# Optimization experiments

Hardware: AMD Instinct MI355X
Metric: run time of the kernel (lower is better)

## Reference

```python
import jax, jax.numpy as jnp
import numpy as np

CONF = 0.25
IOU = 0.7
MAX_DET = 300
IMG_H = 1280
IMG_W = 1280
KPT_SHAPE = (17, 3)
MAX_NMS = 3000
BS = 16
N_ANCH = 33600  # (1280/8)^2 + (1280/16)^2 + (1280/32)^2


def setup_inputs() -> dict:
    key = jax.random.key(0)
    k1, k2, k3, k4 = jax.random.split(key, 4)
    # realistic YOLO head outputs: centers in image, positive w/h, conf in (0,1)
    cxy = jax.random.uniform(k1, (BS, 2, N_ANCH)) * jnp.array([IMG_W, IMG_H], jnp.float32).reshape(1, 2, 1)
    wh = jax.random.uniform(k2, (BS, 2, N_ANCH)) * 200.0 + 4.0
    conf = jax.random.uniform(k3, (BS, 1, N_ANCH))
    kpts = jax.random.uniform(k4, (BS, 51, N_ANCH)) * float(IMG_W)
    preds = jnp.concatenate([cxy, wh, conf, kpts], axis=1).astype(jnp.float32)
    return {"preds": preds}


def _pairwise_iou(boxes):
    # boxes: [M, 4] xyxy
    area = (boxes[:, 2] - boxes[:, 0]) * (boxes[:, 3] - boxes[:, 1])
    lt = jnp.maximum(boxes[:, None, :2], boxes[None, :, :2])
    rb = jnp.minimum(boxes[:, None, 2:], boxes[None, :, 2:])
    wh = jnp.clip(rb - lt, 0.0)
    inter = wh[..., 0] * wh[..., 1]
    return inter / (area[:, None] + area[None, :] - inter + 1e-9)


def _nms_keep(boxes, valid):
    # greedy NMS over score-descending boxes; returns bool keep mask [M]
    M = boxes.shape[0]
    idx = jnp.arange(M)
    supp = (_pairwise_iou(boxes) > IOU) & (idx[None, :] > idx[:, None])

    def body(i, keep):
        # row i suppresses later boxes only if it is itself kept
        return keep & ~(supp[i] & keep[i])

    return jax.lax.fori_loop(0, M, body, valid)


def _per_image(boxes_xywh, scores, kpts):
    # boxes_xywh: [N,4], scores: [N], kpts: [N,51]
    valid = scores > CONF
    masked = jnp.where(valid, scores, -1.0)
    order = jnp.argsort(-masked)[:MAX_NMS]  # top max_nms by score, desc
    b = boxes_xywh[order]
    sc = scores[order]
    kp = kpts[order]
    v = valid[order]
    # xywh -> xyxy with clip to image bounds
    cx, cy, w, h = b[:, 0], b[:, 1], b[:, 2], b[:, 3]
    x1 = jnp.clip(cx - w / 2, 0.0, IMG_W)
    y1 = jnp.clip(cy - h / 2, 0.0, IMG_H)
    x2 = jnp.clip(cx + w / 2, 0.0, IMG_W)
    y2 = jnp.clip(cy + h / 2, 0.0, IMG_H)
    bxy = jnp.stack([x1, y1, x2, y2], axis=-1)
    # faithful to original _clip_coords quirk: only channels 0 and 1 of the 51 clipped
    kp = kp.at[:, 0].set(jnp.clip(kp[:, 0], 0.0, IMG_W))
    kp = kp.at[:, 1].set(jnp.clip(kp[:, 1], 0.0, IMG_H))
    keep = _nms_keep(bxy, v)
    rank = jnp.cumsum(keep) - 1
    sel = keep & (rank < MAX_DET)
    tgt = jnp.where(sel, rank, MAX_DET)  # dropped rows scatter to slot MAX_DET (sliced off)
    ob = jnp.zeros((MAX_DET + 1, 4), bxy.dtype).at[tgt].set(jnp.where(sel[:, None], bxy, 0.0))[:MAX_DET]
    osc = jnp.zeros((MAX_DET + 1, 1), sc.dtype).at[tgt].set(jnp.where(sel[:, None], sc[:, None], 0.0))[:MAX_DET]
    okp = jnp.zeros((MAX_DET + 1, 51), kp.dtype).at[tgt].set(jnp.where(sel[:, None], kp, 0.0))[:MAX_DET]
    return ob, osc, okp


def reference(preds):
    bs = preds.shape[0]
    x = jnp.transpose(preds, (0, 2, 1))  # [bs, N, 56]
    ob, osc, okp = jax.vmap(_per_image)(x[..., :4], x[..., 4], x[..., 5:])
    return ob, osc, okp.reshape(bs, MAX_DET, *KPT_SHAPE)
```

## Files before the change

kernel.cpp:

```cpp
#include <hip/hip_runtime.h>
#include <stdint.h>

#define N_ANCH 33600
#define BS 16
#define NCH 56
#define MAX_NMS 3000
#define MAX_DET 300
#define CONF_T 0.25f
#define IOU_T 0.7f
#define IMG 1280.0f
#define NW 47
#define NBINS 4096
#define HIST_BINS 4097
#define CAP 4096
#define WCAP 4096
#define WC_STRIDE 16

#define OFF_CAND 0
#define OFF_WL   (OFF_CAND + BS*CAP*8)
#define OFF_WC   (OFF_WL + BS*WCAP*4)
#define OFF_KEPT (OFF_WC + BS*WC_STRIDE*4)
#define OFF_OIDX (OFF_KEPT + 64)
#define OFF_SC   (OFF_OIDX + BS*MAX_NMS*4)
#define OFF_SEL  (OFF_SC + BS*MAX_NMS*4)
#define OFF_BOX  (((OFF_SEL + BS*MAX_DET*4) + 15) & ~15)

__device__ __forceinline__ int score_bucket(float c, uint32_t* bits_out) {
    if (!(c > CONF_T)) { *bits_out = 0u; return 0; }
    uint32_t bits = __float_as_uint(c);
    *bits_out = bits;
    int bucket = (int)(bits >> 12) - 0x3E800 + 1;
    bucket = bucket < 1 ? 1 : (bucket > NBINS ? NBINS : bucket);
    return bucket;
}

__global__ void k_phase1(const float* __restrict__ preds,
                         unsigned long long* __restrict__ cand,
                         unsigned int* __restrict__ wlist, int* __restrict__ wcount,
                         int* __restrict__ oidx, float* __restrict__ sc_out,
                         float4* __restrict__ box_out) {
    __shared__ int hl[HIST_BINS];
    __shared__ int st[HIST_BINS];
    __shared__ int part[256];
    __shared__ int suf[256];
    __shared__ int ldsB, ldsM, ldsWc;
    int b = blockIdx.x, t = threadIdx.x;
    if (t == 0) { ldsWc = 0; }
    for (int i = t; i < HIST_BINS; i += 1024) hl[i] = 0;
    __syncthreads();
    const float4* conf4 = (const float4*)(preds + (size_t)b * NCH * N_ANCH + 4 * N_ANCH);
    for (int a4 = t; a4 < N_ANCH / 4; a4 += 1024) {
        float4 c4 = conf4[a4];
        uint32_t bits;
        int bk;
        bk = score_bucket(c4.x, &bits); if (bk > 0) atomicAdd(&hl[bk], 1);
        bk = score_bucket(c4.y, &bits); if (bk > 0) atomicAdd(&hl[bk], 1);
        bk = score_bucket(c4.z, &bits); if (bk > 0) atomicAdd(&hl[bk], 1);
        bk = score_bucket(c4.w, &bits); if (bk > 0) atomicAdd(&hl[bk], 1);
    }
    __syncthreads();
    if (t < 256) {
        int s = 0;
        for (int k = 0; k < 16; k++) s += hl[1 + t * 16 + k];
        part[t] = s;
    }
    __syncthreads();
    if (t == 0) {
        int run = 0;
        for (int i = 255; i >= 0; i--) { suf[i] = run; run += part[i]; }
        if (run < MAX_NMS) { ldsB = 1; ldsM = run; }
    }
    __syncthreads();
    if (t < 256) {
        int run = suf[t];
        bool maycross = (run < MAX_NMS) && (run + part[t] >= MAX_NMS);
        bool done = false;
        for (int k = 15; k >= 0; k--) {
            int bin = 1 + t * 16 + k;
            st[bin] = run;
            run += hl[bin];
            if (maycross && !done && run >= MAX_NMS) { ldsB = bin; ldsM = run; done = true; }
        }
    }
    __syncthreads();
    int B = ldsB, M = ldsM;
    if (t < 256) {
        for (int k = 0; k < 16; k++) {
            int bin = 1 + t * 16 + k;
            int c = hl[bin], s = st[bin];
            if (c > 0 && bin >= B && s < MAX_NMS) {
                int idx = atomicAdd(&ldsWc, 1);
                wlist[b * WCAP + idx] = (unsigned int)s | ((unsigned int)c << 16);
            }
        }
    }
    __syncthreads();
    for (int a4 = t; a4 < N_ANCH / 4; a4 += 1024) {
        float4 c4 = conf4[a4];
        float cv[4] = {c4.x, c4.y, c4.z, c4.w};
        #pragma unroll
        for (int q = 0; q < 4; q++) {
            uint32_t bits;
            int bucket = score_bucket(cv[q], &bits);
            if (bucket >= B && bucket > 0) {
                int pos = atomicAdd(&st[bucket], 1);
                if (pos < CAP) {
                    int a = a4 * 4 + q;
                    cand[b * CAP + pos] =
                        ((unsigned long long)bits << 32) | (uint32_t)(~(uint32_t)a);
                }
            }
        }
    }
    for (int p = M + t; p < MAX_NMS; p += 1024) {
        sc_out[b * MAX_NMS + p] = -1.0f;
        box_out[b * MAX_NMS + p] = make_float4(0.f, 0.f, 0.f, 0.f);
        oidx[b * MAX_NMS + p] = 0;
    }
    if (t == 0) wcount[b * WC_STRIDE] = ldsWc;
}

__global__ void k_rank2(const float* __restrict__ preds,
                        const unsigned long long* __restrict__ cand,
                        const unsigned int* __restrict__ wlist,
                        const int* __restrict__ wcount,
                        int* __restrict__ oidx, float* __restrict__ sc_out,
                        float4* __restrict__ box_out) {
    int b = blockIdx.x;
    int wc = wcount[b * WC_STRIDE];
    int wv = blockIdx.y * (blockDim.x >> 6) + (threadIdx.x >> 6);
    int lane = threadIdx.x & 63;
    const int wstride = gridDim.y * (blockDim.x >> 6);
    const float* pr = preds + (size_t)b * NCH * N_ANCH;
    for (int e = wv; e < wc; e += wstride) {
        unsigned int ent = wlist[b * WCAP + e];
        int s = (int)(ent & 0xffffu);
        int n = (int)(ent >> 16);
        if (s + n > CAP) n = CAP - s;
        const unsigned long long* seg = cand + b * CAP + s;
        for (int i = lane; i < n; i += 64) {
            unsigned long long ke = seg[i];
            int r = 0;
            for (int j = 0; j < n; j++) r += (seg[j] > ke);
            int pos = s + r;
            if (pos < MAX_NMS) {
                int oi = (int)(~(uint32_t)ke);
                float score = __uint_as_float((uint32_t)(ke >> 32));
                float cx = pr[0 * N_ANCH + oi], cy = pr[1 * N_ANCH + oi];
                float w  = pr[2 * N_ANCH + oi], h  = pr[3 * N_ANCH + oi];
                float4 bx;
                bx.x = fminf(fmaxf(cx - w * 0.5f, 0.f), IMG);
                bx.y = fminf(fmaxf(cy - h * 0.5f, 0.f), IMG);
                bx.z = fminf(fmaxf(cx + w * 0.5f, 0.f), IMG);
                bx.w = fminf(fmaxf(cy + h * 0.5f, 0.f), IMG);
                oidx[b * MAX_NMS + pos] = oi;
                sc_out[b * MAX_NMS + pos] = score;
                box_out[b * MAX_NMS + pos] = bx;
            }
        }
    }
}

__device__ __forceinline__ float iou_pair(float4 bi, float ai, float4 bj) {
    float aj  = (bj.z - bj.x) * (bj.w - bj.y);
    float ltx = fmaxf(bi.x, bj.x), lty = fmaxf(bi.y, bj.y);
    float rbx = fminf(bi.z, bj.z), rby = fminf(bi.w, bj.w);
    float wx  = fmaxf(rbx - ltx, 0.f), wy = fmaxf(rby - lty, 0.f);
    float inter = wx * wy;
    return inter / (ai + aj - inter + 1e-9f);
}

__device__ __forceinline__ unsigned long long readlane64(unsigned long long v, int lane) {
    uint32_t lo = (uint32_t)v, hi = (uint32_t)(v >> 32);
    uint32_t rlo = __builtin_amdgcn_readlane(lo, lane);
    uint32_t rhi = __builtin_amdgcn_readlane(hi, lane);
    return ((unsigned long long)rhi << 32) | (unsigned long long)rlo;
}

__global__ void k_nms(const float4* __restrict__ box_ws, const float* __restrict__ sc_ws,
                      int* __restrict__ sel_slot, int* __restrict__ kept_count,
                      float* __restrict__ out) {
    __shared__ float4 lbox[MAX_NMS];
    __shared__ float4 kbox[MAX_DET];
    __shared__ float  karea[MAX_DET];
    __shared__ int    lsel[MAX_DET];
    __shared__ unsigned long long pres[NW];
    __shared__ unsigned long long diag[64];
    __shared__ unsigned long long keptmask_sh;
    int b = blockIdx.x, t = threadIdx.x;
    if (t < NW) pres[t] = 0ull;
    __syncthreads();
    for (int j = t; j < MAX_NMS; j += 1024) {
        lbox[j] = box_ws[b * MAX_NMS + j];
        if (!(sc_ws[b * MAX_NMS + j] > CONF_T))
            atomicOr(&pres[j >> 6], 1ull << (j & 63));
    }
    __syncthreads();
    int kc = 0;
    for (int c = 0; c < NW && kc < MAX_DET; c++) {
        int base = c * 64;
        if (t < 64) diag[t] = 0ull;
        __syncthreads();
        {
            int jl = t >> 4, kk = t & 15;
            int j = base + jl;
            if (j < MAX_NMS && kc > 0) {
                float4 bj = lbox[j];
                bool sup = false;
                for (int kidx = kk; kidx < kc; kidx += 16) {
                    if (iou_pair(kbox[kidx], karea[kidx], bj) > IOU_T) { sup = true; break; }
                }
                if (sup) atomicOr(&pres[c], 1ull << jl);
            }
        }
        {
            int il = t >> 4;
            int j0 = (t & 15) * 4;
            int i = base + il;
            if (i < MAX_NMS) {
                float4 bi = lbox[i];
                float ai = (bi.z - bi.x) * (bi.w - bi.y);
                unsigned long long m = 0ull;
                for (int q = 0; q < 4; q++) {
                    int jl = j0 + q, j = base + jl;
                    if (j > i && j < MAX_NMS) {
                        if (iou_pair(bi, ai, lbox[j]) > IOU_T) m |= 1ull << jl;
                    }
                }
                if (m) atomicOr(&diag[il], m);
            }
        }
        __syncthreads();
        if (t < 64) {
            unsigned long long mydiag = diag[t];
            unsigned long long s = pres[c];
            unsigned long long keptm = 0ull;
            int room = MAX_DET - kc;
            int jmax = MAX_NMS - base; if (jmax > 64) jmax = 64;
            for (int bb = 0; bb < jmax; bb++) {
                if (!((s >> bb) & 1ull)) {
                    s |= readlane64(mydiag, bb);
                    keptm |= 1ull << bb;
                    if (--room == 0) break;
                }
            }
            if (t == 0) keptmask_sh = keptm;
        }
        __syncthreads();
        unsigned long long keptm = keptmask_sh;
        if (t < 64 && ((keptm >> t) & 1ull)) {
            int pos = kc + __popcll(keptm & ((1ull << t) - 1ull));
            float4 bx = lbox[base + t];
            kbox[pos] = bx;
            karea[pos] = (bx.z - bx.x) * (bx.w - bx.y);
            lsel[pos] = base + t;
        }
        kc += __popcll(keptm);
        __syncthreads();
    }
    if (t == 0) kept_count[b] = kc;
    float* ob  = out;
    float* osc = out + BS * MAX_DET * 4;
    for (int r = t; r < MAX_DET; r += 1024) {
        int det = b * MAX_DET + r;
        if (r < kc) {
            float4 bx = kbox[r];
            ob[det * 4 + 0] = bx.x; ob[det * 4 + 1] = bx.y;
            ob[det * 4 + 2] = bx.z; ob[det * 4 + 3] = bx.w;
            osc[det] = sc_ws[b * MAX_NMS + lsel[r]];
            sel_slot[b * MAX_DET + r] = lsel[r];
        } else {
            ob[det * 4 + 0] = 0.f; ob[det * 4 + 1] = 0.f;
            ob[det * 4 + 2] = 0.f; ob[det * 4 + 3] = 0.f;
            osc[det] = 0.f;
        }
    }
}

__global__ void k_kpt(const float* __restrict__ preds, const int* __restrict__ oidx_ws,
                      const int* __restrict__ sel_slot, const int* __restrict__ kept_count,
                      float* __restrict__ out) {
    int g = blockIdx.x * blockDim.x + threadIdx.x;
    int det = g >> 6, lane = g & 63;
    if (det >= BS * MAX_DET || lane >= 51) return;
    int b = det / MAX_DET, r = det - b * MAX_DET;
    float* okp = out + BS * MAX_DET * 5;
    if (r < kept_count[b]) {
        int s = sel_slot[b * MAX_DET + r];
        int oi = oidx_ws[b * MAX_NMS + s];
        float v = preds[(size_t)b * NCH * N_ANCH + (size_t)(5 + lane) * N_ANCH + oi];
        if (lane < 2) v = fminf(fmaxf(v, 0.f), IMG);
        okp[det * 51 + lane] = v;
    } else {
        okp[det * 51 + lane] = 0.f;
    }
}

extern "C" void kernel_launch(void* const* d_in, const int* in_sizes, int n_in,
                              void* d_out, int out_size, void* d_ws, size_t ws_size,
                              hipStream_t stream) {
    const float* preds = (const float*)d_in[0];
    float* out = (float*)d_out;
    char* ws = (char*)d_ws;
    unsigned long long* cand = (unsigned long long*)(ws + OFF_CAND);
    unsigned int* wlist = (unsigned int*)(ws + OFF_WL);
    int* wcount = (int*)(ws + OFF_WC);
    int* kept = (int*)(ws + OFF_KEPT);
    int* oidx = (int*)(ws + OFF_OIDX);
    float* sc = (float*)(ws + OFF_SC);
    int* sel = (int*)(ws + OFF_SEL);
    float4* box = (float4*)(ws + OFF_BOX);

    k_phase1<<<BS, 1024, 0, stream>>>(preds, cand, wlist, wcount, oidx, sc, box);
    k_rank2<<<dim3(BS, 32), 256, 0, stream>>>(preds, cand, wlist, wcount, oidx, sc, box);
    k_nms<<<BS, 1024, 0, stream>>>(box, sc, sel, kept, out);
    k_kpt<<<(BS * MAX_DET * 64 + 255) / 256, 256, 0, stream>>>(preds, oidx, sel, kept, out);
}
```

Baseline: 231.5 us.

## Fuse histogram select, rank, and NMS into one per-image kernel

Merges the candidate histogram, in-bucket ranking, and greedy NMS into a single 1024-thread block per image. Boxes are now written straight into shared memory instead of a global workspace. Score and anchor index are packed into one meta array, and the final anchor index per detection is written out so the keypoint kernel needs a single indirection. This removes two kernel launches and several global round trips. In exchange, the ranking/gather stage runs on only 16 blocks instead of a wider grid, and shared memory is reused by aliasing the histogram region.

```diff
diff --git a/kernel.cpp b/kernel.cpp
--- a/kernel.cpp
+++ b/kernel.cpp
@@ -14,16 +14,11 @@
 #define HIST_BINS 4097
 #define CAP 4096
 #define WCAP 4096
-#define WC_STRIDE 16
 
 #define OFF_CAND 0
 #define OFF_WL   (OFF_CAND + BS*CAP*8)
-#define OFF_WC   (OFF_WL + BS*WCAP*4)
-#define OFF_KEPT (OFF_WC + BS*WC_STRIDE*4)
-#define OFF_OIDX (OFF_KEPT + 64)
-#define OFF_SC   (OFF_OIDX + BS*MAX_NMS*4)
-#define OFF_SEL  (OFF_SC + BS*MAX_NMS*4)
-#define OFF_BOX  (((OFF_SEL + BS*MAX_DET*4) + 15) & ~15)
+#define OFF_META (OFF_WL + BS*WCAP*4)
+#define OFF_FOI  (OFF_META + BS*MAX_NMS*8)
 
 __device__ __forceinline__ int score_bucket(float c, uint32_t* bits_out) {
     if (!(c > CONF_T)) { *bits_out = 0u; return 0; }
@@ -34,20 +29,48 @@
     return bucket;
 }
 
-__global__ void k_phase1(const float* __restrict__ preds,
-                         unsigned long long* __restrict__ cand,
-                         unsigned int* __restrict__ wlist, int* __restrict__ wcount,
-                         int* __restrict__ oidx, float* __restrict__ sc_out,
-                         float4* __restrict__ box_out) {
-    __shared__ int hl[HIST_BINS];
-    __shared__ int st[HIST_BINS];
-    __shared__ int part[256];
-    __shared__ int suf[256];
+__device__ __forceinline__ float iou_pair(float4 bi, float ai, float4 bj) {
+    float aj  = (bj.z - bj.x) * (bj.w - bj.y);
+    float ltx = fmaxf(bi.x, bj.x), lty = fmaxf(bi.y, bj.y);
+    float rbx = fminf(bi.z, bj.z), rby = fminf(bi.w, bj.w);
+    float wx  = fmaxf(rbx - ltx, 0.f), wy = fmaxf(rby - lty, 0.f);
+    float inter = wx * wy;
+    return inter / (ai + aj - inter + 1e-9f);
+}
+
+__device__ __forceinline__ unsigned long long readlane64(unsigned long long v, int lane) {
+    uint32_t lo = (uint32_t)v, hi = (uint32_t)(v >> 32);
+    uint32_t rlo = __builtin_amdgcn_readlane(lo, lane);
+    uint32_t rhi = __builtin_amdgcn_readlane(hi, lane);
+    return ((unsigned long long)rhi << 32) | (unsigned long long)rlo;
+}
+
+__global__ void __launch_bounds__(1024)
+k_fused(const float* __restrict__ preds,
+        unsigned long long* __restrict__ cand,
+        unsigned int* __restrict__ wlist,
+        uint2* __restrict__ meta,
+        int* __restrict__ foi,
+        float* __restrict__ out) {
+    __shared__ __align__(16) char sraw[48000];
+    float4* lbox = (float4*)sraw;
+    int* hl   = (int*)sraw;
+    int* st   = (int*)(sraw + 16388);
+    int* part = (int*)(sraw + 32776);
+    int* suf  = (int*)(sraw + 33800);
+    __shared__ float4 kbox[MAX_DET];
+    __shared__ float  karea[MAX_DET];
+    __shared__ int    lsel[MAX_DET];
+    __shared__ unsigned long long pres[NW];
+    __shared__ unsigned long long diag[64];
+    __shared__ unsigned long long keptmask_sh;
     __shared__ int ldsB, ldsM, ldsWc;
-    int b = blockIdx.x, t = threadIdx.x;
-    if (t == 0) { ldsWc = 0; }
+
+    const int b = blockIdx.x, t = threadIdx.x;
+    if (t == 0) ldsWc = 0;
     for (int i = t; i < HIST_BINS; i += 1024) hl[i] = 0;
     __syncthreads();
+
     const float4* conf4 = (const float4*)(preds + (size_t)b * NCH * N_ANCH + 4 * N_ANCH);
     for (int a4 = t; a4 < N_ANCH / 4; a4 += 1024) {
         float4 c4 = conf4[a4];
@@ -59,6 +82,7 @@
         bk = score_bucket(c4.w, &bits); if (bk > 0) atomicAdd(&hl[bk], 1);
     }
     __syncthreads();
+
     if (t < 256) {
         int s = 0;
         for (int k = 0; k < 16; k++) s += hl[1 + t * 16 + k];
@@ -83,7 +107,8 @@
         }
     }
     __syncthreads();
-    int B = ldsB, M = ldsM;
+    const int B = ldsB, M = ldsM;
+
     if (t < 256) {
         for (int k = 0; k < 16; k++) {
             int bin = 1 + t * 16 + k;
@@ -95,6 +120,7 @@
         }
     }
     __syncthreads();
+
     for (int a4 = t; a4 < N_ANCH / 4; a4 += 1024) {
         float4 c4 = conf4[a4];
         float cv[4] = {c4.x, c4.y, c4.z, c4.w};
@@ -112,90 +138,49 @@
             }
         }
     }
-    for (int p = M + t; p < MAX_NMS; p += 1024) {
-        sc_out[b * MAX_NMS + p] = -1.0f;
-        box_out[b * MAX_NMS + p] = make_float4(0.f, 0.f, 0.f, 0.f);
-        oidx[b * MAX_NMS + p] = 0;
-    }
-    if (t == 0) wcount[b * WC_STRIDE] = ldsWc;
-}
-
-__global__ void k_rank2(const float* __restrict__ preds,
-                        const unsigned long long* __restrict__ cand,
-                        const unsigned int* __restrict__ wlist,
-                        const int* __restrict__ wcount,
-                        int* __restrict__ oidx, float* __restrict__ sc_out,
-                        float4* __restrict__ box_out) {
-    int b = blockIdx.x;
-    int wc = wcount[b * WC_STRIDE];
-    int wv = blockIdx.y * (blockDim.x >> 6) + (threadIdx.x >> 6);
-    int lane = threadIdx.x & 63;
-    const int wstride = gridDim.y * (blockDim.x >> 6);
-    const float* pr = preds + (size_t)b * NCH * N_ANCH;
-    for (int e = wv; e < wc; e += wstride) {
-        unsigned int ent = wlist[b * WCAP + e];
-        int s = (int)(ent & 0xffffu);
-        int n = (int)(ent >> 16);
-        if (s + n > CAP) n = CAP - s;
-        const unsigned long long* seg = cand + b * CAP + s;
-        for (int i = lane; i < n; i += 64) {
-            unsigned long long ke = seg[i];
-            int r = 0;
-            for (int j = 0; j < n; j++) r += (seg[j] > ke);
-            int pos = s + r;
-            if (pos < MAX_NMS) {
-                int oi = (int)(~(uint32_t)ke);
-                float score = __uint_as_float((uint32_t)(ke >> 32));
-                float cx = pr[0 * N_ANCH + oi], cy = pr[1 * N_ANCH + oi];
-                float w  = pr[2 * N_ANCH + oi], h  = pr[3 * N_ANCH + oi];
-                float4 bx;
-                bx.x = fminf(fmaxf(cx - w * 0.5f, 0.f), IMG);
-                bx.y = fminf(fmaxf(cy - h * 0.5f, 0.f), IMG);
-                bx.z = fminf(fmaxf(cx + w * 0.5f, 0.f), IMG);
-                bx.w = fminf(fmaxf(cy + h * 0.5f, 0.f), IMG);
-                oidx[b * MAX_NMS + pos] = oi;
-                sc_out[b * MAX_NMS + pos] = score;
-                box_out[b * MAX_NMS + pos] = bx;
-            }
-        }
-    }
-}
-
-__device__ __forceinline__ float iou_pair(float4 bi, float ai, float4 bj) {
-    float aj  = (bj.z - bj.x) * (bj.w - bj.y);
-    float ltx = fmaxf(bi.x, bj.x), lty = fmaxf(bi.y, bj.y);
-    float rbx = fminf(bi.z, bj.z), rby = fminf(bi.w, bj.w);
-    float wx  = fmaxf(rbx - ltx, 0.f), wy = fmaxf(rby - lty, 0.f);
-    float inter = wx * wy;
-    return inter / (ai + aj - inter + 1e-9f);
-}
-
-__device__ __forceinline__ unsigned long long readlane64(unsigned long long v, int lane) {
-    uint32_t lo = (uint32_t)v, hi = (uint32_t)(v >> 32);
-    uint32_t rlo = __builtin_amdgcn_readlane(lo, lane);
-    uint32_t rhi = __builtin_amdgcn_readlane(hi, lane);
-    return ((unsigned long long)rhi << 32) | (unsigned long long)rlo;
-}
-
-__global__ void k_nms(const float4* __restrict__ box_ws, const float* __restrict__ sc_ws,
-                      int* __restrict__ sel_slot, int* __restrict__ kept_count,
-                      float* __restrict__ out) {
-    __shared__ float4 lbox[MAX_NMS];
-    __shared__ float4 kbox[MAX_DET];
-    __shared__ float  karea[MAX_DET];
-    __shared__ int    lsel[MAX_DET];
-    __shared__ unsigned long long pres[NW];
-    __shared__ unsigned long long diag[64];
-    __shared__ unsigned long long keptmask_sh;
-    int b = blockIdx.x, t = threadIdx.x;
-    if (t < NW) pres[t] = 0ull;
-    __syncthreads();
-    for (int j = t; j < MAX_NMS; j += 1024) {
-        lbox[j] = box_ws[b * MAX_NMS + j];
-        if (!(sc_ws[b * MAX_NMS + j] > CONF_T))
-            atomicOr(&pres[j >> 6], 1ull << (j & 63));
-    }
-    __syncthreads();
+    __syncthreads();
+
+    for (int p = M + t; p < MAX_NMS; p += 1024) lbox[p] = make_float4(0.f, 0.f, 0.f, 0.f);
+    if (t < NW) {
+        int base = t * 64;
+        int lo = M - base;
+        unsigned long long inv = (lo <= 0) ? ~0ull : (lo >= 64 ? 0ull : ~((1ull << lo) - 1ull));
+        pres[t] = inv;
+    }
+
+    {
+        const int wv = t >> 6, lane = t & 63;
+        const int wc = ldsWc;
+        const float* pr = preds + (size_t)b * NCH * N_ANCH;
+        for (int e = wv; e < wc; e += 16) {
+            unsigned int ent = wlist[b * WCAP + e];
+            int s = (int)(ent & 0xffffu);
+            int n = (int)(ent >> 16);
+            if (s + n > CAP) n = CAP - s;
+            const unsigned long long* seg = cand + b * CAP + s;
+            for (int i = lane; i < n; i += 64) {
+                unsigned long long ke = seg[i];
+                int r = 0;
+                for (int j = 0; j < n; j++) r += (seg[j] > ke);
+                int pos = s + r;
+                if (pos < MAX_NMS) {
+                    int oi = (int)(~(uint32_t)ke);
+                    uint32_t sbits = (uint32_t)(ke >> 32);
+                    float cx = pr[0 * N_ANCH + oi], cy = pr[1 * N_ANCH + oi];
+                    float w  = pr[2 * N_ANCH + oi], h  = pr[3 * N_ANCH + oi];
+                    float4 bx;
+                    bx.x = fminf(fmaxf(cx - w * 0.5f, 0.f), IMG);
+                    bx.y = fminf(fmaxf(cy - h * 0.5f, 0.f), IMG);
+                    bx.z = fminf(fmaxf(cx + w * 0.5f, 0.f), IMG);
+                    bx.w = fminf(fmaxf(cy + h * 0.5f, 0.f), IMG);
+                    lbox[pos] = bx;
+                    meta[b * MAX_NMS + pos] = make_uint2((unsigned int)oi, sbits);
+                }
+            }
+        }
+    }
+    __syncthreads();
+
     int kc = 0;
     for (int c = 0; c < NW && kc < MAX_DET; c++) {
         int base = c * 64;
@@ -258,7 +243,7 @@
         kc += __popcll(keptm);
         __syncthreads();
     }
-    if (t == 0) kept_count[b] = kc;
+
     float* ob  = out;
     float* osc = out + BS * MAX_DET * 4;
     for (int r = t; r < MAX_DET; r += 1024) {
@@ -267,27 +252,27 @@
             float4 bx = kbox[r];
             ob[det * 4 + 0] = bx.x; ob[det * 4 + 1] = bx.y;
             ob[det * 4 + 2] = bx.z; ob[det * 4 + 3] = bx.w;
-            osc[det] = sc_ws[b * MAX_NMS + lsel[r]];
-            sel_slot[b * MAX_DET + r] = lsel[r];
+            uint2 mt = meta[b * MAX_NMS + lsel[r]];
+            osc[det] = __uint_as_float(mt.y);
+            foi[det] = (int)mt.x;
         } else {
             ob[det * 4 + 0] = 0.f; ob[det * 4 + 1] = 0.f;
             ob[det * 4 + 2] = 0.f; ob[det * 4 + 3] = 0.f;
             osc[det] = 0.f;
-        }
-    }
-}
-
-__global__ void k_kpt(const float* __restrict__ preds, const int* __restrict__ oidx_ws,
-                      const int* __restrict__ sel_slot, const int* __restrict__ kept_count,
+            foi[det] = -1;
+        }
+    }
+}
+
+__global__ void k_kpt(const float* __restrict__ preds, const int* __restrict__ foi,
                       float* __restrict__ out) {
     int g = blockIdx.x * blockDim.x + threadIdx.x;
     int det = g >> 6, lane = g & 63;
     if (det >= BS * MAX_DET || lane >= 51) return;
-    int b = det / MAX_DET, r = det - b * MAX_DET;
+    int b = det / MAX_DET;
     float* okp = out + BS * MAX_DET * 5;
-    if (r < kept_count[b]) {
-        int s = sel_slot[b * MAX_DET + r];
-        int oi = oidx_ws[b * MAX_NMS + s];
+    int oi = foi[det];
+    if (oi >= 0) {
         float v = preds[(size_t)b * NCH * N_ANCH + (size_t)(5 + lane) * N_ANCH + oi];
         if (lane < 2) v = fminf(fmaxf(v, 0.f), IMG);
         okp[det * 51 + lane] = v;
@@ -304,15 +289,9 @@
     char* ws = (char*)d_ws;
     unsigned long long* cand = (unsigned long long*)(ws + OFF_CAND);
     unsigned int* wlist = (unsigned int*)(ws + OFF_WL);
-    int* wcount = (int*)(ws + OFF_WC);
-    int* kept = (int*)(ws + OFF_KEPT);
-    int* oidx = (int*)(ws + OFF_OIDX);
-    float* sc = (float*)(ws + OFF_SC);
-    int* sel = (int*)(ws + OFF_SEL);
-    float4* box = (float4*)(ws + OFF_BOX);
-
-    k_phase1<<<BS, 1024, 0, stream>>>(preds, cand, wlist, wcount, oidx, sc, box);
-    k_rank2<<<dim3(BS, 32), 256, 0, stream>>>(preds, cand, wlist, wcount, oidx, sc, box);
-    k_nms<<<BS, 1024, 0, stream>>>(box, sc, sel, kept, out);
-    k_kpt<<<(BS * MAX_DET * 64 + 255) / 256, 256, 0, stream>>>(preds, oidx, sel, kept, out);
-}
+    uint2* meta = (uint2*)(ws + OFF_META);
+    int* foi = (int*)(ws + OFF_FOI);
+
+    k_fused<<<BS, 1024, 0, stream>>>(preds, cand, wlist, meta, foi, out);
+    k_kpt<<<(BS * MAX_DET * 64 + 255) / 256, 256, 0, stream>>>(preds, foi, out);
+}
```

Result: slower. 305.2 us (+31.8%).
